# Performance work log

Measured on AMD Instinct MI355X. Metric: run time of the kernel, lower is better.

The kernel has to match this reference:

```python
import jax, jax.numpy as jnp
from jax import lax
import numpy as np

D_MODEL = 512
D_STATE = 16
D_CONV = 4
EXPAND = 2
D_INNER = EXPAND * D_MODEL  # 1024
DT_RANK = (D_MODEL + 15) // 16  # 32
FF_DIM = 1024
N_LAYERS = 2
B, L = 2, 2048


def setup_inputs() -> dict:
    key = jax.random.key(0)
    ks = jax.random.split(key, 16)
    s = 0.02
    x = jax.random.normal(ks[0], (B, L, D_MODEL), jnp.float32)
    in_proj_w = jax.random.normal(ks[1], (N_LAYERS, 2 * D_INNER, D_MODEL), jnp.float32) * s
    conv_w = jax.random.normal(ks[2], (N_LAYERS, D_INNER, D_CONV), jnp.float32) * 0.3
    conv_b = jax.random.normal(ks[3], (N_LAYERS, D_INNER), jnp.float32) * s
    x_proj_w = jax.random.normal(ks[4], (N_LAYERS, DT_RANK + 2 * D_STATE, D_INNER), jnp.float32) * s
    dt_proj_w = jax.random.normal(ks[5], (N_LAYERS, D_INNER, DT_RANK), jnp.float32) * s
    dt_proj_b = jax.random.normal(ks[6], (N_LAYERS, D_INNER), jnp.float32) * 0.5 - 4.0
    A_log = jnp.log(jnp.broadcast_to(jnp.arange(1, D_STATE + 1, dtype=jnp.float32), (N_LAYERS, D_INNER, D_STATE)))
    Dp = jnp.ones((N_LAYERS, D_INNER), jnp.float32)
    out_proj_w = jax.random.normal(ks[7], (N_LAYERS, D_MODEL, D_INNER), jnp.float32) * s
    mlp_w1 = jax.random.normal(ks[8], (FF_DIM, D_MODEL), jnp.float32) * s
    mlp_b1 = jnp.zeros((FF_DIM,), jnp.float32)
    mlp_w2 = jax.random.normal(ks[9], (D_MODEL, FF_DIM), jnp.float32) * s
    mlp_b2 = jnp.zeros((D_MODEL,), jnp.float32)
    return dict(x=x, in_proj_w=in_proj_w, conv_w=conv_w, conv_b=conv_b,
                x_proj_w=x_proj_w, dt_proj_w=dt_proj_w, dt_proj_b=dt_proj_b,
                A_log=A_log, Dp=Dp, out_proj_w=out_proj_w,
                mlp_w1=mlp_w1, mlp_b1=mlp_b1, mlp_w2=mlp_w2, mlp_b2=mlp_b2)


def _mamba_layer(x, ipw, cw, cb, xpw, dpw, dpb, Al, Dv, opw):
    # x: [B, L, d_model]
    b, l, _ = x.shape
    xz = jnp.einsum('bld,ed->ble', x, ipw)           # [B, L, 2*d_inner]
    xin, z = jnp.split(xz, 2, axis=-1)
    # causal depthwise conv1d (pad left d_conv-1)
    xc = jnp.transpose(xin, (0, 2, 1))               # [B, d_inner, L]
    xc = lax.conv_general_dilated(xc, cw[:, None, :], (1,), [(D_CONV - 1, 0)],
                                  feature_group_count=D_INNER)
    xin = jax.nn.silu(jnp.transpose(xc + cb[:, None], (0, 2, 1)))  # [B, L, d_inner]
    dbl = jnp.einsum('bld,ed->ble', xin, xpw)        # [B, L, dt_rank + 2*d_state]
    dt, Bm, Cm = jnp.split(dbl, [DT_RANK, DT_RANK + D_STATE], axis=-1)
    dt = jax.nn.softplus(jnp.einsum('blr,dr->bld', dt, dpw) + dpb)  # [B, L, d_inner]
    A = -jnp.exp(Al)                                  # [d_inner, d_state]
    dA = jnp.exp(dt[..., None] * A)                   # [B, L, d_inner, d_state]
    dBu = dt[..., None] * Bm[:, :, None, :] * xin[..., None]

    def step(h, inp):
        dA_t, dBu_t = inp
        h = dA_t * h + dBu_t
        return h, h

    h0 = jnp.zeros((b, D_INNER, D_STATE), x.dtype)
    _, hs = lax.scan(step, h0, (jnp.moveaxis(dA, 1, 0), jnp.moveaxis(dBu, 1, 0)))
    hs = jnp.moveaxis(hs, 0, 1)                       # [B, L, d_inner, d_state]
    y = jnp.einsum('blds,bls->bld', hs, Cm) + xin * Dv
    y = y * jax.nn.silu(z)
    return jnp.einsum('ble,de->bld', y, opw)


def reference(x, in_proj_w, conv_w, conv_b, x_proj_w, dt_proj_w, dt_proj_b,
              A_log, Dp, out_proj_w, mlp_w1, mlp_b1, mlp_w2, mlp_b2):
    residual = x
    for i in range(N_LAYERS):
        x = _mamba_layer(x, in_proj_w[i], conv_w[i], conv_b[i], x_proj_w[i],
                         dt_proj_w[i], dt_proj_b[i], A_log[i], Dp[i], out_proj_w[i])
    h = x + residual
    h = jax.nn.relu(jnp.einsum('bld,fd->blf', h, mlp_w1) + mlp_b1)  # dropout is identity in eval
    return jnp.einsum('blf,df->bld', h, mlp_w2) + mlp_b2
```

## Files before the change

kernel.cpp:

```cpp
#include <hip/hip_runtime.h>
#include <hip/hip_bf16.h>

#define BB 2
#define LL 2048
#define DMODEL 512
#define DSTATE 16
#define DINNER 1024
#define DTRANK 32
#define FFDIM 1024
#define MTOT (BB*LL)
#define SCL 64
#define NCC 32

typedef unsigned short u16;
typedef __attribute__((ext_vector_type(8))) short bf16x8;
typedef __attribute__((ext_vector_type(4))) float f32x4;

__device__ __forceinline__ float b2f(u16 u){
  unsigned v = ((unsigned)u) << 16; float f; __builtin_memcpy(&f, &v, 4); return f;
}
__device__ __forceinline__ u16 f2b(float f){
  unsigned u; __builtin_memcpy(&u, &f, 4);
  unsigned r = (u + 0x7FFFu + ((u >> 16) & 1u)) >> 16;
  return (u16)r;
}
__device__ __forceinline__ float siluf(float x){ return x / (1.f + __expf(-x)); }

__device__ __forceinline__ float ldin(const void* p, size_t i, int bf){
  if (bf) return b2f(((const u16*)p)[i]);
  return ((const float*)p)[i];
}
__device__ __forceinline__ void stout(void* p, size_t i, int bf, float v){
  if (bf) ((u16*)p)[i] = f2b(v);
  else    ((float*)p)[i] = v;
}

__device__ __forceinline__ int getbf(const void* dp){
  return (*(const unsigned*)dp == 0x3F803F80u) ? 1 : 0;
}

#define CVT_X   (MTOT*DMODEL)
#define CVT_IPW (2*2*DINNER*DMODEL)
#define CVT_XPW (2*64*DINNER)
#define CVT_DPW (2*DINNER*DTRANK)
#define CVT_OPW (2*DMODEL*DINNER)
#define CVT_W1  (FFDIM*DMODEL)
#define CVT_W2  (DMODEL*FFDIM)
#define CVT_TOT (CVT_X+CVT_IPW+CVT_XPW+CVT_DPW+CVT_OPW+CVT_W1+CVT_W2)
__global__ __launch_bounds__(256) void cvt_all_k(
    const void* __restrict__ x, const void* __restrict__ ipw,
    const void* __restrict__ xpw, const void* __restrict__ dpw,
    const void* __restrict__ opw, const void* __restrict__ w1,
    const void* __restrict__ w2, u16* __restrict__ dst,
    const void* __restrict__ dprobe)
{
  const int bf = getbf(dprobe);
  size_t i4 = ((size_t)blockIdx.x * 256 + threadIdx.x) * 4;
  if (i4 >= CVT_TOT) return;
  const void* src; size_t off = i4;
  if      (off < CVT_X)                       { src = x; }
  else if ((off -= CVT_X)   < CVT_IPW)        { src = ipw; }
  else if ((off -= CVT_IPW) < CVT_XPW)        { src = xpw; }
  else if ((off -= CVT_XPW) < CVT_DPW)        { src = dpw; }
  else if ((off -= CVT_DPW) < CVT_OPW)        { src = opw; }
  else if ((off -= CVT_OPW) < CVT_W1)         { src = w1; }
  else     { off -= CVT_W1;                     src = w2; }
  ushort4 o;
  if (bf) {
    o = *(const ushort4*)((const u16*)src + off);
  } else {
    float4 f = *(const float4*)((const float*)src + off);
    o.x = f2b(f.x); o.y = f2b(f.y); o.z = f2b(f.z); o.w = f2b(f.w);
  }
  *(ushort4*)(dst + i4) = o;
}

template<int CVT>
__device__ __forceinline__ bf16x8 ld8(const void* P, size_t gi, int bf){
  if (!CVT || bf) return *(const bf16x8*)((const u16*)P + gi);
  float4 f0 = *(const float4*)((const float*)P + gi);
  float4 f1 = *(const float4*)((const float*)P + gi + 4);
  union { u16 u[8]; bf16x8 v; } t;
  t.u[0]=f2b(f0.x); t.u[1]=f2b(f0.y); t.u[2]=f2b(f0.z); t.u[3]=f2b(f0.w);
  t.u[4]=f2b(f1.x); t.u[5]=f2b(f1.y); t.u[6]=f2b(f1.z); t.u[7]=f2b(f1.w);
  return t.v;
}

template<int ACT, int AIN, int CIN, int BM, int BN, int FST, int RESID>
__global__ __launch_bounds__(256) void gemm_mfma(
    const void* __restrict__ A, size_t aoff, int lda,
    const void* __restrict__ W, size_t woff,
    const void* __restrict__ bias, size_t boff,
    void* __restrict__ C, size_t coff, int ldc, int K,
    const void* __restrict__ xres, size_t xroff,
    const void* __restrict__ dprobe)
{
  const int bf = getbf(dprobe);
  constexpr int AL = BM / 64, WL = BN / 64;
  constexpr int CVTA = (!FST && AIN) ? 1 : 0;
  constexpr int CVTW = (!FST) ? 1 : 0;
  __shared__ __align__(16) u16 As[2][BM * 32];
  __shared__ __align__(16) u16 Ws[2][BN * 32];
  const int tid = threadIdx.x;
  const int row0 = blockIdx.y * BM, col0 = blockIdx.x * BN;
  const int wave = tid >> 6, lane = tid & 63;
  const int l15 = lane & 15, quad = lane >> 4;
  constexpr int WMT = (BM == 64) ? 1 : ((BN == 128) ? 4 : 2);
  const int mbase = (BM == 64) ? (wave * 16)
                  : ((BN == 128) ? (wave & 1) * 64 : wave * 32);
  const int nbase = (BM == 128 && BN == 128) ? (wave >> 1) * 64 : 0;

  const int rT = tid >> 2, csw = tid & 3;
  const int scg = csw ^ ((rT >> 1) & 3);
  const int lws = rT * 32 + csw * 8;
  const size_t ab0 = aoff + (size_t)(row0 + rT) * lda + scg * 8;
  const size_t wb0 = woff + (size_t)(col0 + rT) * K   + scg * 8;

  f32x4 acc[WMT][4];
#pragma unroll
  for (int i = 0; i < WMT; i++)
#pragma unroll
    for (int j = 0; j < 4; j++) acc[i][j] = (f32x4){0.f,0.f,0.f,0.f};

  const int NT = K >> 5;
  bf16x8 ra0[AL], rw0[WL], ra1[AL], rw1[WL];

#define GLOAD(RA, RW, T) do { const int k1_ = (T) * 32;                        \
  _Pragma("unroll") for (int i = 0; i < AL; i++)                               \
    RA[i] = ld8<CVTA>(A, ab0 + k1_ + (size_t)i * 64 * lda, bf);                \
  _Pragma("unroll") for (int i = 0; i < WL; i++)                               \
    RW[i] = ld8<CVTW>(W, wb0 + k1_ + (size_t)i * 64 * K, bf); } while (0)

#define GSTEP(RA, RW, T) do {                                                  \
  const int cur_ = (T) & 1;                                                    \
  _Pragma("unroll") for (int i = 0; i < AL; i++)                               \
    *(bf16x8*)&As[cur_][i * 2048 + lws] = RA[i];                               \
  _Pragma("unroll") for (int i = 0; i < WL; i++)                               \
    *(bf16x8*)&Ws[cur_][i * 2048 + lws] = RW[i];                               \
  if ((T) + 2 < NT) GLOAD(RA, RW, (T) + 2);                                    \
  __syncthreads();                                                             \
  bf16x8 af_[WMT], bf_[4];                                                     \
  _Pragma("unroll") for (int mt = 0; mt < WMT; mt++) {                         \
    int r_ = mbase + mt * 16 + l15;                                            \
    af_[mt] = *(const bf16x8*)&As[cur_][r_ * 32 + ((quad ^ ((r_ >> 1) & 3)) << 3)]; } \
  _Pragma("unroll") for (int nt = 0; nt < 4; nt++) {                           \
    int r_ = nbase + nt * 16 + l15;                                            \
    bf_[nt] = *(const bf16x8*)&Ws[cur_][r_ * 32 + ((quad ^ ((r_ >> 1) & 3)) << 3)]; } \
  _Pragma("unroll") for (int mt = 0; mt < WMT; mt++)                           \
    _Pragma("unroll") for (int nt = 0; nt < 4; nt++)                           \
      acc[mt][nt] = __builtin_amdgcn_mfma_f32_16x16x32_bf16(af_[mt], bf_[nt], acc[mt][nt], 0, 0, 0); \
} while (0)

  GLOAD(ra0, rw0, 0);
  if (NT > 1) GLOAD(ra1, rw1, 1);
  int t = 0;
  for (; t + 1 < NT; t += 2) { GSTEP(ra0, rw0, t); GSTEP(ra1, rw1, t + 1); }
  if (t < NT) GSTEP(ra0, rw0, t);
#undef GLOAD
#undef GSTEP

#pragma unroll
  for (int nt = 0; nt < 4; nt++) {
    int c = col0 + nbase + nt * 16 + l15;
    float bv = bias ? ldin(bias, boff + c, bf) : 0.f;
#pragma unroll
    for (int mt = 0; mt < WMT; mt++) {
      int rb = row0 + mbase + mt * 16 + quad * 4;
#pragma unroll
      for (int r = 0; r < 4; r++) {
        float v = acc[mt][nt][r] + bv;
        if (ACT == 1) v = fmaxf(v, 0.f) + __logf(1.f + __expf(-fabsf(v)));
        if (ACT == 2) v = fmaxf(v, 0.f);
        size_t ci = (size_t)(rb + r) * ldc + c;
        if (RESID) v += ldin(xres, xroff + ci, bf);
        if (CIN) stout(C, coff + ci, bf, v);
        else     ((u16*)C)[coff + ci] = f2b(v);
      }
    }
  }
}

__global__ __launch_bounds__(256) void conv_k(
    const u16* __restrict__ xz, const void* __restrict__ cw, size_t cwo,
    const void* __restrict__ cb, size_t cbo, u16* __restrict__ xc,
    const void* __restrict__ dprobe)
{
  const int bf = getbf(dprobe);
  int idx = blockIdx.x * 256 + threadIdx.x;
  int d = idx & 1023;
  int row = idx >> 10;
  int lb = row & (LL - 1);
  float acc = ldin(cb, cbo + d, bf);
#pragma unroll
  for (int k = 0; k < 4; k++) {
    int lk = lb - 3 + k;
    if (lk >= 0) acc += ldin(cw, cwo + d*4 + k, bf) * b2f(xz[(size_t)(row - 3 + k) * 2048 + d]);
  }
  xc[idx] = f2b(siluf(acc));
}

__global__ __launch_bounds__(256) void scan_A_k(
    const u16* __restrict__ dtp, int sdt, const u16* __restrict__ xc,
    const u16* __restrict__ dbl, const void* __restrict__ Alog, size_t alo,
    float* __restrict__ Pc, float* __restrict__ Sc, const void* __restrict__ dprobe)
{
  const int bf = getbf(dprobe);
  int bid = blockIdx.x;
  int b = bid >> 9;
  int c = (bid >> 4) & (NCC - 1);
  int g = bid & 15;
  int t = threadIdx.x;
  int dl = t >> 2, sq = t & 3;
  int d0 = g * 64, d = d0 + dl;
  int rowb = b * LL + c * SCL;

  __shared__ __align__(16) u16 dts[64 * 64];
  __shared__ __align__(16) u16 us[64 * 64];
  __shared__ __align__(16) float Bs[64 * 20];
#pragma unroll
  for (int p = 0; p < 2; p++) {
    int seg = p * 256 + t;
    int r = seg >> 3, c8 = (seg & 7) * 8;
    bf16x8 dv = *(const bf16x8*)&dtp[(size_t)(rowb + r) * sdt + d0 + c8];
    bf16x8 uv = *(const bf16x8*)&xc[(size_t)(rowb + r) * 1024 + d0 + c8];
    int coff = r >> 3, roff = r & 7;
#pragma unroll
    for (int i = 0; i < 8; i++) {
      int dd = c8 + i;
      int idx = dd * 64 + ((coff ^ (dd & 7)) << 3) + roff;
      dts[idx] = (u16)dv[i];
      us[idx]  = (u16)uv[i];
    }
  }
  if (t < 128) {
    int l = t >> 1, grp = t & 1;
    bf16x8 v = *(const bf16x8*)&dbl[(size_t)(rowb + l) * 64 + 32 + grp * 8];
    f32x4 f0 = {b2f((u16)v[0]), b2f((u16)v[1]), b2f((u16)v[2]), b2f((u16)v[3])};
    f32x4 f1 = {b2f((u16)v[4]), b2f((u16)v[5]), b2f((u16)v[6]), b2f((u16)v[7])};
    *(f32x4*)&Bs[l * 20 + grp * 8]     = f0;
    *(f32x4*)&Bs[l * 20 + grp * 8 + 4] = f1;
  }
  float Av[4];
#pragma unroll
  for (int j = 0; j < 4; j++)
    Av[j] = -__expf(ldin(Alog, alo + (size_t)d * DSTATE + sq * 4 + j, bf));
  __syncthreads();

  float h[4] = {0.f,0.f,0.f,0.f}, P[4] = {1.f,1.f,1.f,1.f};
  for (int cc = 0; cc < 8; cc++) {
    int base = dl * 64 + ((cc ^ (dl & 7)) << 3);
    bf16x8 dt8 = *(const bf16x8*)&dts[base];
    bf16x8 u8  = *(const bf16x8*)&us[base];
#pragma unroll
    for (int i = 0; i < 8; i++) {
      int l = cc * 8 + i;
      float dtv = b2f((u16)dt8[i]);
      float uv  = b2f((u16)u8[i]);
      float dtu = dtv * uv;
      f32x4 B4 = *(const f32x4*)&Bs[l * 20 + sq * 4];
#pragma unroll
      for (int j = 0; j < 4; j++) {
        float dA = __expf(dtv * Av[j]);
        h[j] = dA * h[j] + dtu * B4[j];
        P[j] *= dA;
      }
    }
  }
  size_t o = (((size_t)b * DINNER + d) * NCC + c) * DSTATE + sq * 4;
  *(f32x4*)&Pc[o] = (f32x4){P[0], P[1], P[2], P[3]};
  *(f32x4*)&Sc[o] = (f32x4){h[0], h[1], h[2], h[3]};
}

__global__ __launch_bounds__(256) void scan_B_k(
    float* __restrict__ Pc, const float* __restrict__ Sc)
{
  int idx = blockIdx.x * 256 + threadIdx.x;
  int bd = idx >> 4, s = idx & 15;
  float h = 0.f;
  for (int c = 0; c < NCC; c++) {
    size_t o = ((size_t)bd * NCC + c) * DSTATE + s;
    float P = Pc[o], S = Sc[o];
    Pc[o] = h;
    h = P * h + S;
  }
}

__global__ __launch_bounds__(256) void scan_C_k(
    u16* __restrict__ dtp, int sdt, const u16* __restrict__ xz,
    const u16* __restrict__ xc,
    const u16* __restrict__ dbl, const void* __restrict__ Alog, size_t alo,
    const void* __restrict__ Dpt, size_t dpo, const float* __restrict__ Hinit,
    const void* __restrict__ dprobe)
{
  const int bf = getbf(dprobe);
  int bid = blockIdx.x;
  int b = bid >> 9;
  int c = (bid >> 4) & (NCC - 1);
  int g = bid & 15;
  int t = threadIdx.x;
  int dl = t >> 2, sq = t & 3;
  int d0 = g * 64, d = d0 + dl;
  int rowb = b * LL + c * SCL;

  __shared__ __align__(16) u16 dts[64 * 64];
  __shared__ __align__(16) u16 us[64 * 64];
  __shared__ __align__(16) u16 outs[64 * 64];
  __shared__ __align__(16) float BCs[64 * 36];
#pragma unroll
  for (int p = 0; p < 2; p++) {
    int seg = p * 256 + t;
    int r = seg >> 3, c8 = (seg & 7) * 8;
    bf16x8 dv = *(const bf16x8*)&dtp[(size_t)(rowb + r) * sdt + d0 + c8];
    bf16x8 uv = *(const bf16x8*)&xc[(size_t)(rowb + r) * 1024 + d0 + c8];
    int coff = r >> 3, roff = r & 7;
#pragma unroll
    for (int i = 0; i < 8; i++) {
      int dd = c8 + i;
      int idx = dd * 64 + ((coff ^ (dd & 7)) << 3) + roff;
      dts[idx] = (u16)dv[i];
      us[idx]  = (u16)uv[i];
    }
  }
  {
    int l = t >> 2, grp = t & 3;
    bf16x8 v = *(const bf16x8*)&dbl[(size_t)(rowb + l) * 64 + 32 + grp * 8];
    f32x4 f0 = {b2f((u16)v[0]), b2f((u16)v[1]), b2f((u16)v[2]), b2f((u16)v[3])};
    f32x4 f1 = {b2f((u16)v[4]), b2f((u16)v[5]), b2f((u16)v[6]), b2f((u16)v[7])};
    *(f32x4*)&BCs[l * 36 + grp * 8]     = f0;
    *(f32x4*)&BCs[l * 36 + grp * 8 + 4] = f1;
  }
  float Av[4];
#pragma unroll
  for (int j = 0; j < 4; j++)
    Av[j] = -__expf(ldin(Alog, alo + (size_t)d * DSTATE + sq * 4 + j, bf));
  float Dv = ldin(Dpt, dpo + d, bf);
  float h[4];
  size_t o = (((size_t)b * DINNER + d) * NCC + c) * DSTATE + sq * 4;
  f32x4 h4 = *(const f32x4*)&Hinit[o];
  h[0] = h4[0]; h[1] = h4[1]; h[2] = h4[2]; h[3] = h4[3];
  __syncthreads();

  for (int cc = 0; cc < 8; cc++) {
    int base = dl * 64 + ((cc ^ (dl & 7)) << 3);
    bf16x8 dt8 = *(const bf16x8*)&dts[base];
    bf16x8 u8  = *(const bf16x8*)&us[base];
#pragma unroll
    for (int i = 0; i < 8; i++) {
      int l = cc * 8 + i;
      float dtv = b2f((u16)dt8[i]);
      float uv  = b2f((u16)u8[i]);
      float dtu = dtv * uv;
      f32x4 B4 = *(const f32x4*)&BCs[l * 36 + sq * 4];
      f32x4 C4 = *(const f32x4*)&BCs[l * 36 + 16 + sq * 4];
      float y = 0.f;
#pragma unroll
      for (int j = 0; j < 4; j++) {
        float dA = __expf(dtv * Av[j]);
        h[j] = dA * h[j] + dtu * B4[j];
        y += h[j] * C4[j];
      }
      y += __shfl_xor(y, 1);
      y += __shfl_xor(y, 2);
      if (sq == 0) outs[l * 64 + dl] = f2b(y + uv * Dv);
    }
  }
  __syncthreads();
#pragma unroll
  for (int p = 0; p < 2; p++) {
    int seg = p * 256 + t;
    int r = seg >> 3, c8 = (seg & 7) * 8;
    bf16x8 yv = *(const bf16x8*)&outs[r * 64 + c8];
    bf16x8 zv = *(const bf16x8*)&xz[(size_t)(rowb + r) * 2048 + 1024 + d0 + c8];
    bf16x8 ov;
#pragma unroll
    for (int i = 0; i < 8; i++) {
      float z = b2f((u16)zv[i]);
      ov[i] = (short)f2b(b2f((u16)yv[i]) * siluf(z));
    }
    *(bf16x8*)&dtp[(size_t)(rowb + r) * sdt + d0 + c8] = ov;
  }
}

extern "C" void kernel_launch(void* const* d_in, const int* in_sizes, int n_in,
                              void* d_out, int out_size, void* d_ws, size_t ws_size,
                              hipStream_t stream) {
  const void* x_in = d_in[0];
  const void* ipw  = d_in[1];
  const void* cw   = d_in[2];
  const void* cb   = d_in[3];
  const void* xpw  = d_in[4];
  const void* dpw  = d_in[5];
  const void* dpb  = d_in[6];
  const void* Alog = d_in[7];
  const void* Dpt  = d_in[8];
  const void* opw  = d_in[9];
  const void* w1   = d_in[10];
  const void* b1   = d_in[11];
  const void* w2   = d_in[12];
  const void* b2   = d_in[13];

  const bool full = ws_size >= (size_t)64 * 1024 * 1024;

  if (full) {
    float* Pc = (float*)((char*)d_ws + 64);
    float* Sc = Pc + (size_t)BB*DINNER*NCC*DSTATE;
    u16* p = (u16*)(Sc + (size_t)BB*DINNER*NCC*DSTATE);
    u16* x16   = p;  p += (size_t)CVT_X;
    u16* ipw16 = p;  p += (size_t)CVT_IPW;
    u16* xpw16 = p;  p += (size_t)CVT_XPW;
    u16* dpw16 = p;  p += (size_t)CVT_DPW;
    u16* opw16 = p;  p += (size_t)CVT_OPW;
    u16* w116  = p;  p += (size_t)CVT_W1;
    u16* w216  = p;  p += (size_t)CVT_W2;
    u16* xz    = p;  p += (size_t)MTOT*2*DINNER;
    u16* xc    = p;  p += (size_t)MTOT*DINNER;
    u16* dty   = p;  p += (size_t)MTOT*DINNER;
    u16* dbl   = p;
    u16* bx = xc;
    u16* resid = xz;
    u16* hid = xz + (size_t)4*1024*1024;

    cvt_all_k<<<(CVT_TOT/4 + 255)/256, 256, 0, stream>>>(
        x_in, ipw, xpw, dpw, opw, w1, w2, x16, Dpt);

    for (int layer = 0; layer < 2; layer++) {
      size_t ipw_o = (size_t)layer*2*DINNER*DMODEL;
      size_t cw_o  = (size_t)layer*DINNER*4,  cb_o = (size_t)layer*DINNER;
      size_t xpw_o = (size_t)layer*64*DINNER, dpw_o = (size_t)layer*DINNER*DTRANK;
      size_t dpb_o = (size_t)layer*DINNER,    al_o = (size_t)layer*DINNER*DSTATE;
      size_t dp_o  = (size_t)layer*DINNER,    opw_o = (size_t)layer*DMODEL*DINNER;
      const u16* xsrc = (layer == 0) ? x16 : bx;
      gemm_mfma<0,0,0,128,128,1,0><<<dim3(16, 32), 256, 0, stream>>>(
          xsrc, 0, DMODEL, ipw16, ipw_o, nullptr, 0, xz, 0, 2048, DMODEL,
          nullptr, 0, Dpt);
      conv_k<<<MTOT*DINNER/256, 256, 0, stream>>>(xz, cw, cw_o, cb, cb_o, xc, Dpt);
      gemm_mfma<0,0,0,64,64,1,0><<<dim3(1, 64), 256, 0, stream>>>(
          xc, 0, DINNER, xpw16, xpw_o, nullptr, 0, dbl, 0, 64, DINNER,
          nullptr, 0, Dpt);
      gemm_mfma<1,0,0,64,64,1,0><<<dim3(16, 64), 256, 0, stream>>>(
          dbl, 0, 64, dpw16, dpw_o, dpb, dpb_o, dty, 0, 1024, DTRANK,
          nullptr, 0, Dpt);
      scan_A_k<<<BB*NCC*16, 256, 0, stream>>>(dty, 1024, xc, dbl, Alog, al_o, Pc, Sc, Dpt);
      scan_B_k<<<BB*64, 256, 0, stream>>>(Pc, Sc);
      scan_C_k<<<BB*NCC*16, 256, 0, stream>>>(dty, 1024, xz, xc, dbl, Alog, al_o,
                                              Dpt, dp_o, Pc, Dpt);
      if (layer == 0)
        gemm_mfma<0,0,0,64,64,1,0><<<dim3(8, 64), 256, 0, stream>>>(
            dty, 0, 1024, opw16, opw_o, nullptr, 0, bx, 0, DMODEL, DINNER,
            nullptr, 0, Dpt);
      else
        gemm_mfma<0,0,0,64,64,1,1><<<dim3(8, 64), 256, 0, stream>>>(
            dty, 0, 1024, opw16, opw_o, nullptr, 0, resid, 0, DMODEL, DINNER,
            x_in, 0, Dpt);
    }
    gemm_mfma<2,0,0,64,64,1,0><<<dim3(16, 64), 256, 0, stream>>>(
        resid, 0, DMODEL, w116, 0, b1, 0, hid, 0, FFDIM, DMODEL,
        nullptr, 0, Dpt);
    gemm_mfma<0,0,1,64,64,1,0><<<dim3(8, 64), 256, 0, stream>>>(
        hid, 0, FFDIM, w216, 0, b2, 0, d_out, 0, DMODEL, FFDIM,
        nullptr, 0, Dpt);
  } else {
    float* Pc = (float*)((char*)d_ws + 64);
    float* Sc = Pc + (size_t)DINNER*NCC*DSTATE;
    u16* p = (u16*)(Sc + (size_t)DINNER*NCC*DSTATE);
    u16* xz  = p;  p += (size_t)LL*2*DINNER;
    u16* xc  = p;  p += (size_t)LL*DINNER;
    u16* bxF = p;  p += (size_t)MTOT*DMODEL;
    u16* dbl = p;
    u16* hid = xz + (size_t)2*1024*1024;

    for (int layer = 0; layer < 2; layer++) {
      size_t ipw_o = (size_t)layer*2*DINNER*DMODEL;
      size_t cw_o  = (size_t)layer*DINNER*4,  cb_o = (size_t)layer*DINNER;
      size_t xpw_o = (size_t)layer*64*DINNER, dpw_o = (size_t)layer*DINNER*DTRANK;
      size_t dpb_o = (size_t)layer*DINNER,    al_o = (size_t)layer*DINNER*DSTATE;
      size_t dp_o  = (size_t)layer*DINNER,    opw_o = (size_t)layer*DMODEL*DINNER;
      for (int b = 0; b < BB; b++) {
        size_t ro = (size_t)b * LL * DMODEL;
        if (layer == 0)
          gemm_mfma<0,1,0,128,128,0,0><<<dim3(16, 16), 256, 0, stream>>>(
              x_in, ro, DMODEL, ipw, ipw_o, nullptr, 0, xz, 0, 2048, DMODEL,
              nullptr, 0, Dpt);
        else
          gemm_mfma<0,0,0,128,128,0,0><<<dim3(16, 16), 256, 0, stream>>>(
              bxF, ro, DMODEL, ipw, ipw_o, nullptr, 0, xz, 0, 2048, DMODEL,
              nullptr, 0, Dpt);
        conv_k<<<LL*DINNER/256, 256, 0, stream>>>(xz, cw, cw_o, cb, cb_o, xc, Dpt);
        gemm_mfma<0,0,0,64,64,0,0><<<dim3(1, 32), 256, 0, stream>>>(
            xc, 0, DINNER, xpw, xpw_o, nullptr, 0, dbl, 0, 64, DINNER,
            nullptr, 0, Dpt);
        gemm_mfma<1,0,0,64,64,0,0><<<dim3(16, 32), 256, 0, stream>>>(
            dbl, 0, 64, dpw, dpw_o, dpb, dpb_o, xz, 0, 2048, DTRANK,
            nullptr, 0, Dpt);
        scan_A_k<<<NCC*16, 256, 0, stream>>>(xz, 2048, xc, dbl, Alog, al_o, Pc, Sc, Dpt);
        scan_B_k<<<64, 256, 0, stream>>>(Pc, Sc);
        scan_C_k<<<NCC*16, 256, 0, stream>>>(xz, 2048, xz, xc, dbl, Alog, al_o,
                                             Dpt, dp_o, Pc, Dpt);
        if (layer == 0)
          gemm_mfma<0,0,0,64,64,0,0><<<dim3(8, 32), 256, 0, stream>>>(
              xz, 0, 2048, opw, opw_o, nullptr, 0, bxF, ro, DMODEL, DINNER,
              nullptr, 0, Dpt);
        else
          gemm_mfma<0,0,0,64,64,0,1><<<dim3(8, 32), 256, 0, stream>>>(
              xz, 0, 2048, opw, opw_o, nullptr, 0, bxF, ro, DMODEL, DINNER,
              x_in, ro, Dpt);
      }
    }
    for (int b = 0; b < BB; b++) {
      size_t ro = (size_t)b * LL * DMODEL;
      gemm_mfma<2,0,0,64,64,0,0><<<dim3(16, 32), 256, 0, stream>>>(
          bxF, ro, DMODEL, w1, 0, b1, 0, hid, 0, FFDIM, DMODEL,
          nullptr, 0, Dpt);
      gemm_mfma<0,0,1,64,64,0,0><<<dim3(8, 32), 256, 0, stream>>>(
          hid, 0, FFDIM, w2, 0, b2, 0, d_out, ro, DMODEL, FFDIM,
          nullptr, 0, Dpt);
    }
  }
}
```

Measured before the change: 357.0 us.

## Fuse dt_proj GEMM and softplus into scan kernels, vectorize conv, drop x conversion

Result: faster. 328.9 us (-7.9%).

```diff
diff --git a/kernel.cpp b/kernel.cpp
--- a/kernel.cpp
+++ b/kernel.cpp
@@ -25,6 +25,9 @@
   return (u16)r;
 }
 __device__ __forceinline__ float siluf(float x){ return x / (1.f + __expf(-x)); }
+__device__ __forceinline__ float softplusf(float v){
+  return fmaxf(v, 0.f) + __logf(1.f + __expf(-fabsf(v)));
+}
 
 __device__ __forceinline__ float ldin(const void* p, size_t i, int bf){
   if (bf) return b2f(((const u16*)p)[i]);
@@ -37,42 +40,6 @@
 
 __device__ __forceinline__ int getbf(const void* dp){
   return (*(const unsigned*)dp == 0x3F803F80u) ? 1 : 0;
-}
-
-#define CVT_X   (MTOT*DMODEL)
-#define CVT_IPW (2*2*DINNER*DMODEL)
-#define CVT_XPW (2*64*DINNER)
-#define CVT_DPW (2*DINNER*DTRANK)
-#define CVT_OPW (2*DMODEL*DINNER)
-#define CVT_W1  (FFDIM*DMODEL)
-#define CVT_W2  (DMODEL*FFDIM)
-#define CVT_TOT (CVT_X+CVT_IPW+CVT_XPW+CVT_DPW+CVT_OPW+CVT_W1+CVT_W2)
-__global__ __launch_bounds__(256) void cvt_all_k(
-    const void* __restrict__ x, const void* __restrict__ ipw,
-    const void* __restrict__ xpw, const void* __restrict__ dpw,
-    const void* __restrict__ opw, const void* __restrict__ w1,
-    const void* __restrict__ w2, u16* __restrict__ dst,
-    const void* __restrict__ dprobe)
-{
-  const int bf = getbf(dprobe);
-  size_t i4 = ((size_t)blockIdx.x * 256 + threadIdx.x) * 4;
-  if (i4 >= CVT_TOT) return;
-  const void* src; size_t off = i4;
-  if      (off < CVT_X)                       { src = x; }
-  else if ((off -= CVT_X)   < CVT_IPW)        { src = ipw; }
-  else if ((off -= CVT_IPW) < CVT_XPW)        { src = xpw; }
-  else if ((off -= CVT_XPW) < CVT_DPW)        { src = dpw; }
-  else if ((off -= CVT_DPW) < CVT_OPW)        { src = opw; }
-  else if ((off -= CVT_OPW) < CVT_W1)         { src = w1; }
-  else     { off -= CVT_W1;                     src = w2; }
-  ushort4 o;
-  if (bf) {
-    o = *(const ushort4*)((const u16*)src + off);
-  } else {
-    float4 f = *(const float4*)((const float*)src + off);
-    o.x = f2b(f.x); o.y = f2b(f.y); o.z = f2b(f.z); o.w = f2b(f.w);
-  }
-  *(ushort4*)(dst + i4) = o;
 }
 
 template<int CVT>
@@ -86,7 +53,45 @@
   return t.v;
 }
 
-template<int ACT, int AIN, int CIN, int BM, int BN, int FST, int RESID>
+#define CVT_IPW (2*2*DINNER*DMODEL)
+#define CVT_XPW (2*64*DINNER)
+#define CVT_DPW (2*DINNER*DTRANK)
+#define CVT_OPW (2*DMODEL*DINNER)
+#define CVT_W1  (FFDIM*DMODEL)
+#define CVT_W2  (DMODEL*FFDIM)
+#define CVT_CW  (2*DINNER*4)
+#define CVT_CB  (2*DINNER)
+#define CVT_TOT (CVT_IPW+CVT_XPW+CVT_DPW+CVT_OPW+CVT_W1+CVT_W2+CVT_CW+CVT_CB)
+__global__ __launch_bounds__(256) void cvt_all_k(
+    const void* __restrict__ ipw, const void* __restrict__ xpw,
+    const void* __restrict__ dpw, const void* __restrict__ opw,
+    const void* __restrict__ w1, const void* __restrict__ w2,
+    const void* __restrict__ cw, const void* __restrict__ cb,
+    u16* __restrict__ dst, const void* __restrict__ dprobe)
+{
+  const int bf = getbf(dprobe);
+  size_t i4 = ((size_t)blockIdx.x * 256 + threadIdx.x) * 4;
+  if (i4 >= CVT_TOT) return;
+  const void* src; size_t off = i4;
+  if      (off < CVT_IPW)                     { src = ipw; }
+  else if ((off -= CVT_IPW) < CVT_XPW)        { src = xpw; }
+  else if ((off -= CVT_XPW) < CVT_DPW)        { src = dpw; }
+  else if ((off -= CVT_DPW) < CVT_OPW)        { src = opw; }
+  else if ((off -= CVT_OPW) < CVT_W1)         { src = w1; }
+  else if ((off -= CVT_W1)  < CVT_W2)         { src = w2; }
+  else if ((off -= CVT_W2)  < CVT_CW)         { src = cw; }
+  else     { off -= CVT_CW;                     src = cb; }
+  ushort4 o;
+  if (bf) {
+    o = *(const ushort4*)((const u16*)src + off);
+  } else {
+    float4 f = *(const float4*)((const float*)src + off);
+    o.x = f2b(f.x); o.y = f2b(f.y); o.z = f2b(f.z); o.w = f2b(f.w);
+  }
+  *(ushort4*)(dst + i4) = o;
+}
+
+template<int ACT, int CVA, int CVW, int CIN, int BM, int BN, int RESID>
 __global__ __launch_bounds__(256) void gemm_mfma(
     const void* __restrict__ A, size_t aoff, int lda,
     const void* __restrict__ W, size_t woff,
@@ -97,8 +102,6 @@
 {
   const int bf = getbf(dprobe);
   constexpr int AL = BM / 64, WL = BN / 64;
-  constexpr int CVTA = (!FST && AIN) ? 1 : 0;
-  constexpr int CVTW = (!FST) ? 1 : 0;
   __shared__ __align__(16) u16 As[2][BM * 32];
   __shared__ __align__(16) u16 Ws[2][BN * 32];
   const int tid = threadIdx.x;
@@ -127,9 +130,9 @@
 
 #define GLOAD(RA, RW, T) do { const int k1_ = (T) * 32;                        \
   _Pragma("unroll") for (int i = 0; i < AL; i++)                               \
-    RA[i] = ld8<CVTA>(A, ab0 + k1_ + (size_t)i * 64 * lda, bf);                \
+    RA[i] = ld8<CVA>(A, ab0 + k1_ + (size_t)i * 64 * lda, bf);                 \
   _Pragma("unroll") for (int i = 0; i < WL; i++)                               \
-    RW[i] = ld8<CVTW>(W, wb0 + k1_ + (size_t)i * 64 * K, bf); } while (0)
+    RW[i] = ld8<CVW>(W, wb0 + k1_ + (size_t)i * 64 * K, bf); } while (0)
 
 #define GSTEP(RA, RW, T) do {                                                  \
   const int cur_ = (T) & 1;                                                    \
@@ -169,7 +172,7 @@
 #pragma unroll
       for (int r = 0; r < 4; r++) {
         float v = acc[mt][nt][r] + bv;
-        if (ACT == 1) v = fmaxf(v, 0.f) + __logf(1.f + __expf(-fabsf(v)));
+        if (ACT == 1) v = softplusf(v);
         if (ACT == 2) v = fmaxf(v, 0.f);
         size_t ci = (size_t)(rb + r) * ldc + c;
         if (RESID) v += ldin(xres, xroff + ci, bf);
@@ -180,29 +183,70 @@
   }
 }
 
+template<int FST>
 __global__ __launch_bounds__(256) void conv_k(
     const u16* __restrict__ xz, const void* __restrict__ cw, size_t cwo,
     const void* __restrict__ cb, size_t cbo, u16* __restrict__ xc,
     const void* __restrict__ dprobe)
 {
-  const int bf = getbf(dprobe);
-  int idx = blockIdx.x * 256 + threadIdx.x;
-  int d = idx & 1023;
-  int row = idx >> 10;
-  int lb = row & (LL - 1);
-  float acc = ldin(cb, cbo + d, bf);
-#pragma unroll
-  for (int k = 0; k < 4; k++) {
-    int lk = lb - 3 + k;
-    if (lk >= 0) acc += ldin(cw, cwo + d*4 + k, bf) * b2f(xz[(size_t)(row - 3 + k) * 2048 + d]);
-  }
-  xc[idx] = f2b(siluf(acc));
-}
-
+  if (FST) {
+    const u16* cw16 = (const u16*)cw;
+    const u16* cb16 = (const u16*)cb;
+    int idx8 = (blockIdx.x * 256 + threadIdx.x) * 8;
+    int d8 = idx8 & 1023;
+    int row = idx8 >> 10;
+    int lb = row & (LL - 1);
+    bf16x8 cwv0 = *(const bf16x8*)&cw16[cwo + d8*4];
+    bf16x8 cwv1 = *(const bf16x8*)&cw16[cwo + d8*4 + 8];
+    bf16x8 cwv2 = *(const bf16x8*)&cw16[cwo + d8*4 + 16];
+    bf16x8 cwv3 = *(const bf16x8*)&cw16[cwo + d8*4 + 24];
+    bf16x8 cbv  = *(const bf16x8*)&cb16[cbo + d8];
+    bf16x8 xv0 = (bf16x8){0,0,0,0,0,0,0,0}, xv1 = xv0, xv2 = xv0, xv3 = xv0;
+    if (lb >= 3) xv0 = *(const bf16x8*)&xz[(size_t)(row - 3) * 2048 + d8];
+    if (lb >= 2) xv1 = *(const bf16x8*)&xz[(size_t)(row - 2) * 2048 + d8];
+    if (lb >= 1) xv2 = *(const bf16x8*)&xz[(size_t)(row - 1) * 2048 + d8];
+    xv3 = *(const bf16x8*)&xz[(size_t)row * 2048 + d8];
+    bf16x8 ov;
+#pragma unroll
+    for (int i = 0; i < 8; i++) {
+      float acc = b2f((u16)cbv[i]);
+      int c0 = i * 4;
+      float w0 = b2f((u16)((c0 < 8) ? cwv0[c0 & 7] : (c0 < 16) ? cwv1[c0 & 7] : (c0 < 24) ? cwv2[c0 & 7] : cwv3[c0 & 7]));
+      float w1_ = b2f((u16)(((c0+1) < 8) ? cwv0[(c0+1) & 7] : ((c0+1) < 16) ? cwv1[(c0+1) & 7] : ((c0+1) < 24) ? cwv2[(c0+1) & 7] : cwv3[(c0+1) & 7]));
+      float w2_ = b2f((u16)(((c0+2) < 8) ? cwv0[(c0+2) & 7] : ((c0+2) < 16) ? cwv1[(c0+2) & 7] : ((c0+2) < 24) ? cwv2[(c0+2) & 7] : cwv3[(c0+2) & 7]));
+      float w3_ = b2f((u16)(((c0+3) < 8) ? cwv0[(c0+3) & 7] : ((c0+3) < 16) ? cwv1[(c0+3) & 7] : ((c0+3) < 24) ? cwv2[(c0+3) & 7] : cwv3[(c0+3) & 7]));
+      acc += w0 * b2f((u16)xv0[i]);
+      acc += w1_ * b2f((u16)xv1[i]);
+      acc += w2_ * b2f((u16)xv2[i]);
+      acc += w3_ * b2f((u16)xv3[i]);
+      ov[i] = (short)f2b(siluf(acc));
+    }
+    *(bf16x8*)&xc[idx8] = ov;
+  } else {
+    const int bf = getbf(dprobe);
+    int idx = blockIdx.x * 256 + threadIdx.x;
+    int d = idx & 1023;
+    int row = idx >> 10;
+    int lb = row & (LL - 1);
+    float acc = ldin(cb, cbo + d, bf);
+#pragma unroll
+    for (int k = 0; k < 4; k++) {
+      int lk = lb - 3 + k;
+      if (lk >= 0) acc += ldin(cw, cwo + d*4 + k, bf) * b2f(xz[(size_t)(row - 3 + k) * 2048 + d]);
+    }
+    xc[idx] = f2b(siluf(acc));
+  }
+}
+
+template<int CVW>
 __global__ __launch_bounds__(256) void scan_A_k(
-    const u16* __restrict__ dtp, int sdt, const u16* __restrict__ xc,
-    const u16* __restrict__ dbl, const void* __restrict__ Alog, size_t alo,
-    float* __restrict__ Pc, float* __restrict__ Sc, const void* __restrict__ dprobe)
+    const u16* __restrict__ xc,
+    const u16* __restrict__ dbl,
+    const void* __restrict__ dpwp, size_t dpwo,
+    const void* __restrict__ dpbp, size_t dpbo,
+    const void* __restrict__ Alog, size_t alo,
+    float* __restrict__ Pc, float* __restrict__ Sc,
+    const void* __restrict__ dprobe)
 {
   const int bf = getbf(dprobe);
   int bid = blockIdx.x;
@@ -217,19 +261,26 @@
   __shared__ __align__(16) u16 dts[64 * 64];
   __shared__ __align__(16) u16 us[64 * 64];
   __shared__ __align__(16) float Bs[64 * 20];
+  u16* dbls = dts;
+  u16* dpws = dts + 64 * 32;
+
+  {
+    int r = t >> 2, c8 = (t & 3) * 8;
+    *(bf16x8*)&dbls[r * 32 + c8] =
+        *(const bf16x8*)&dbl[(size_t)(rowb + r) * 64 + c8];
+    *(bf16x8*)&dpws[r * 32 + c8] =
+        ld8<CVW>(dpwp, dpwo + (size_t)(d0 + r) * DTRANK + c8, bf);
+  }
 #pragma unroll
   for (int p = 0; p < 2; p++) {
     int seg = p * 256 + t;
     int r = seg >> 3, c8 = (seg & 7) * 8;
-    bf16x8 dv = *(const bf16x8*)&dtp[(size_t)(rowb + r) * sdt + d0 + c8];
     bf16x8 uv = *(const bf16x8*)&xc[(size_t)(rowb + r) * 1024 + d0 + c8];
     int coff = r >> 3, roff = r & 7;
 #pragma unroll
     for (int i = 0; i < 8; i++) {
       int dd = c8 + i;
-      int idx = dd * 64 + ((coff ^ (dd & 7)) << 3) + roff;
-      dts[idx] = (u16)dv[i];
-      us[idx]  = (u16)uv[i];
+      us[dd * 64 + ((coff ^ (dd & 7)) << 3) + roff] = (u16)uv[i];
     }
   }
   if (t < 128) {
@@ -244,6 +295,36 @@
 #pragma unroll
   for (int j = 0; j < 4; j++)
     Av[j] = -__expf(ldin(Alog, alo + (size_t)d * DSTATE + sq * 4 + j, bf));
+  __syncthreads();
+
+  {
+    int wv = t >> 6, lane = t & 63;
+    int fl = lane & 15, qd = lane >> 4;
+    bf16x8 afr  = *(const bf16x8*)&dbls[(wv * 16 + fl) * 32 + qd * 8];
+    bf16x8 bfr0 = *(const bf16x8*)&dpws[(fl)      * 32 + qd * 8];
+    bf16x8 bfr1 = *(const bf16x8*)&dpws[(16 + fl) * 32 + qd * 8];
+    bf16x8 bfr2 = *(const bf16x8*)&dpws[(32 + fl) * 32 + qd * 8];
+    bf16x8 bfr3 = *(const bf16x8*)&dpws[(48 + fl) * 32 + qd * 8];
+    __syncthreads();
+    f32x4 zz = {0.f, 0.f, 0.f, 0.f};
+    f32x4 a0 = __builtin_amdgcn_mfma_f32_16x16x32_bf16(afr, bfr0, zz, 0, 0, 0);
+    f32x4 a1 = __builtin_amdgcn_mfma_f32_16x16x32_bf16(afr, bfr1, zz, 0, 0, 0);
+    f32x4 a2 = __builtin_amdgcn_mfma_f32_16x16x32_bf16(afr, bfr2, zz, 0, 0, 0);
+    f32x4 a3 = __builtin_amdgcn_mfma_f32_16x16x32_bf16(afr, bfr3, zz, 0, 0, 0);
+    int lc = wv * 2 + (qd >> 1);
+    int off = (qd & 1) * 4;
+#define DTWR(AN, NT) do {                                                      \
+    int dd_ = (NT) * 16 + fl;                                                  \
+    float bvv_ = ldin(dpbp, dpbo + d0 + dd_, bf);                              \
+    ushort4 pk_;                                                               \
+    pk_.x = f2b(softplusf(AN[0] + bvv_));                                      \
+    pk_.y = f2b(softplusf(AN[1] + bvv_));                                      \
+    pk_.z = f2b(softplusf(AN[2] + bvv_));                                      \
+    pk_.w = f2b(softplusf(AN[3] + bvv_));                                      \
+    *(ushort4*)&dts[dd_ * 64 + ((lc ^ (dd_ & 7)) << 3) + off] = pk_; } while (0)
+    DTWR(a0, 0); DTWR(a1, 1); DTWR(a2, 2); DTWR(a3, 3);
+#undef DTWR
+  }
   __syncthreads();
 
   float h[4] = {0.f,0.f,0.f,0.f}, P[4] = {1.f,1.f,1.f,1.f};
@@ -285,10 +366,14 @@
   }
 }
 
+template<int CVW>
 __global__ __launch_bounds__(256) void scan_C_k(
     u16* __restrict__ dtp, int sdt, const u16* __restrict__ xz,
     const u16* __restrict__ xc,
-    const u16* __restrict__ dbl, const void* __restrict__ Alog, size_t alo,
+    const u16* __restrict__ dbl,
+    const void* __restrict__ dpwp, size_t dpwo,
+    const void* __restrict__ dpbp, size_t dpbo,
+    const void* __restrict__ Alog, size_t alo,
     const void* __restrict__ Dpt, size_t dpo, const float* __restrict__ Hinit,
     const void* __restrict__ dprobe)
 {
@@ -306,19 +391,26 @@
   __shared__ __align__(16) u16 us[64 * 64];
   __shared__ __align__(16) u16 outs[64 * 64];
   __shared__ __align__(16) float BCs[64 * 36];
+  u16* dbls = dts;
+  u16* dpws = dts + 64 * 32;
+
+  {
+    int r = t >> 2, c8 = (t & 3) * 8;
+    *(bf16x8*)&dbls[r * 32 + c8] =
+        *(const bf16x8*)&dbl[(size_t)(rowb + r) * 64 + c8];
+    *(bf16x8*)&dpws[r * 32 + c8] =
+        ld8<CVW>(dpwp, dpwo + (size_t)(d0 + r) * DTRANK + c8, bf);
+  }
 #pragma unroll
   for (int p = 0; p < 2; p++) {
     int seg = p * 256 + t;
     int r = seg >> 3, c8 = (seg & 7) * 8;
-    bf16x8 dv = *(const bf16x8*)&dtp[(size_t)(rowb + r) * sdt + d0 + c8];
     bf16x8 uv = *(const bf16x8*)&xc[(size_t)(rowb + r) * 1024 + d0 + c8];
     int coff = r >> 3, roff = r & 7;
 #pragma unroll
     for (int i = 0; i < 8; i++) {
       int dd = c8 + i;
-      int idx = dd * 64 + ((coff ^ (dd & 7)) << 3) + roff;
-      dts[idx] = (u16)dv[i];
-      us[idx]  = (u16)uv[i];
+      us[dd * 64 + ((coff ^ (dd & 7)) << 3) + roff] = (u16)uv[i];
     }
   }
   {
@@ -338,6 +430,36 @@
   size_t o = (((size_t)b * DINNER + d) * NCC + c) * DSTATE + sq * 4;
   f32x4 h4 = *(const f32x4*)&Hinit[o];
   h[0] = h4[0]; h[1] = h4[1]; h[2] = h4[2]; h[3] = h4[3];
+  __syncthreads();
+
+  {
+    int wv = t >> 6, lane = t & 63;
+    int fl = lane & 15, qd = lane >> 4;
+    bf16x8 afr  = *(const bf16x8*)&dbls[(wv * 16 + fl) * 32 + qd * 8];
+    bf16x8 bfr0 = *(const bf16x8*)&dpws[(fl)      * 32 + qd * 8];
+    bf16x8 bfr1 = *(const bf16x8*)&dpws[(16 + fl) * 32 + qd * 8];
+    bf16x8 bfr2 = *(const bf16x8*)&dpws[(32 + fl) * 32 + qd * 8];
+    bf16x8 bfr3 = *(const bf16x8*)&dpws[(48 + fl) * 32 + qd * 8];
+    __syncthreads();
+    f32x4 zz = {0.f, 0.f, 0.f, 0.f};
+    f32x4 a0 = __builtin_amdgcn_mfma_f32_16x16x32_bf16(afr, bfr0, zz, 0, 0, 0);
+    f32x4 a1 = __builtin_amdgcn_mfma_f32_16x16x32_bf16(afr, bfr1, zz, 0, 0, 0);
+    f32x4 a2 = __builtin_amdgcn_mfma_f32_16x16x32_bf16(afr, bfr2, zz, 0, 0, 0);
+    f32x4 a3 = __builtin_amdgcn_mfma_f32_16x16x32_bf16(afr, bfr3, zz, 0, 0, 0);
+    int lc = wv * 2 + (qd >> 1);
+    int off = (qd & 1) * 4;
+#define DTWR(AN, NT) do {                                                      \
+    int dd_ = (NT) * 16 + fl;                                                  \
+    float bvv_ = ldin(dpbp, dpbo + d0 + dd_, bf);                              \
+    ushort4 pk_;                                                               \
+    pk_.x = f2b(softplusf(AN[0] + bvv_));                                      \
+    pk_.y = f2b(softplusf(AN[1] + bvv_));                                      \
+    pk_.z = f2b(softplusf(AN[2] + bvv_));                                      \
+    pk_.w = f2b(softplusf(AN[3] + bvv_));                                      \
+    *(ushort4*)&dts[dd_ * 64 + ((lc ^ (dd_ & 7)) << 3) + off] = pk_; } while (0)
+    DTWR(a0, 0); DTWR(a1, 1); DTWR(a2, 2); DTWR(a3, 3);
+#undef DTWR
+  }
   __syncthreads();
 
   for (int cc = 0; cc < 8; cc++) {
@@ -405,13 +527,15 @@
     float* Pc = (float*)((char*)d_ws + 64);
     float* Sc = Pc + (size_t)BB*DINNER*NCC*DSTATE;
     u16* p = (u16*)(Sc + (size_t)BB*DINNER*NCC*DSTATE);
-    u16* x16   = p;  p += (size_t)CVT_X;
+    u16* cvt0  = p;
     u16* ipw16 = p;  p += (size_t)CVT_IPW;
     u16* xpw16 = p;  p += (size_t)CVT_XPW;
     u16* dpw16 = p;  p += (size_t)CVT_DPW;
     u16* opw16 = p;  p += (size_t)CVT_OPW;
     u16* w116  = p;  p += (size_t)CVT_W1;
     u16* w216  = p;  p += (size_t)CVT_W2;
+    u16* cw16  = p;  p += (size_t)CVT_CW;
+    u16* cb16  = p;  p += (size_t)CVT_CB;
     u16* xz    = p;  p += (size_t)MTOT*2*DINNER;
     u16* xc    = p;  p += (size_t)MTOT*DINNER;
     u16* dty   = p;  p += (size_t)MTOT*DINNER;
@@ -421,7 +545,7 @@
     u16* hid = xz + (size_t)4*1024*1024;
 
     cvt_all_k<<<(CVT_TOT/4 + 255)/256, 256, 0, stream>>>(
-        x_in, ipw, xpw, dpw, opw, w1, w2, x16, Dpt);
+        ipw, xpw, dpw, opw, w1, w2, cw, cb, cvt0, Dpt);
 
     for (int layer = 0; layer < 2; layer++) {
       size_t ipw_o = (size_t)layer*2*DINNER*DMODEL;
@@ -429,34 +553,38 @@
       size_t xpw_o = (size_t)layer*64*DINNER, dpw_o = (size_t)layer*DINNER*DTRANK;
       size_t dpb_o = (size_t)layer*DINNER,    al_o = (size_t)layer*DINNER*DSTATE;
       size_t dp_o  = (size_t)layer*DINNER,    opw_o = (size_t)layer*DMODEL*DINNER;
-      const u16* xsrc = (layer == 0) ? x16 : bx;
-      gemm_mfma<0,0,0,128,128,1,0><<<dim3(16, 32), 256, 0, stream>>>(
-          xsrc, 0, DMODEL, ipw16, ipw_o, nullptr, 0, xz, 0, 2048, DMODEL,
-          nullptr, 0, Dpt);
-      conv_k<<<MTOT*DINNER/256, 256, 0, stream>>>(xz, cw, cw_o, cb, cb_o, xc, Dpt);
-      gemm_mfma<0,0,0,64,64,1,0><<<dim3(1, 64), 256, 0, stream>>>(
+      if (layer == 0)
+        gemm_mfma<0,1,0,0,128,128,0><<<dim3(16, 32), 256, 0, stream>>>(
+            x_in, 0, DMODEL, ipw16, ipw_o, nullptr, 0, xz, 0, 2048, DMODEL,
+            nullptr, 0, Dpt);
+      else
+        gemm_mfma<0,0,0,0,128,128,0><<<dim3(16, 32), 256, 0, stream>>>(
+            bx, 0, DMODEL, ipw16, ipw_o, nullptr, 0, xz, 0, 2048, DMODEL,
+            nullptr, 0, Dpt);
+      conv_k<1><<<MTOT*DINNER/2048, 256, 0, stream>>>(
+          xz, cw16, cw_o, cb16, cb_o, xc, Dpt);
+      gemm_mfma<0,0,0,0,64,64,0><<<dim3(1, 64), 256, 0, stream>>>(
           xc, 0, DINNER, xpw16, xpw_o, nullptr, 0, dbl, 0, 64, DINNER,
           nullptr, 0, Dpt);
-      gemm_mfma<1,0,0,64,64,1,0><<<dim3(16, 64), 256, 0, stream>>>(
-          dbl, 0, 64, dpw16, dpw_o, dpb, dpb_o, dty, 0, 1024, DTRANK,
-          nullptr, 0, Dpt);
-      scan_A_k<<<BB*NCC*16, 256, 0, stream>>>(dty, 1024, xc, dbl, Alog, al_o, Pc, Sc, Dpt);
+      scan_A_k<0><<<BB*NCC*16, 256, 0, stream>>>(
+          xc, dbl, dpw16, dpw_o, dpb, dpb_o, Alog, al_o, Pc, Sc, Dpt);
       scan_B_k<<<BB*64, 256, 0, stream>>>(Pc, Sc);
-      scan_C_k<<<BB*NCC*16, 256, 0, stream>>>(dty, 1024, xz, xc, dbl, Alog, al_o,
-                                              Dpt, dp_o, Pc, Dpt);
+      scan_C_k<0><<<BB*NCC*16, 256, 0, stream>>>(
+          dty, 1024, xz, xc, dbl, dpw16, dpw_o, dpb, dpb_o, Alog, al_o,
+          Dpt, dp_o, Pc, Dpt);
       if (layer == 0)
-        gemm_mfma<0,0,0,64,64,1,0><<<dim3(8, 64), 256, 0, stream>>>(
+        gemm_mfma<0,0,0,0,64,64,0><<<dim3(8, 64), 256, 0, stream>>>(
             dty, 0, 1024, opw16, opw_o, nullptr, 0, bx, 0, DMODEL, DINNER,
             nullptr, 0, Dpt);
       else
-        gemm_mfma<0,0,0,64,64,1,1><<<dim3(8, 64), 256, 0, stream>>>(
+        gemm_mfma<0,0,0,0,64,64,1><<<dim3(8, 64), 256, 0, stream>>>(
             dty, 0, 1024, opw16, opw_o, nullptr, 0, resid, 0, DMODEL, DINNER,
             x_in, 0, Dpt);
     }
-    gemm_mfma<2,0,0,64,64,1,0><<<dim3(16, 64), 256, 0, stream>>>(
+    gemm_mfma<2,0,0,0,64,64,0><<<dim3(16, 64), 256, 0, stream>>>(
         resid, 0, DMODEL, w116, 0, b1, 0, hid, 0, FFDIM, DMODEL,
         nullptr, 0, Dpt);
-    gemm_mfma<0,0,1,64,64,1,0><<<dim3(8, 64), 256, 0, stream>>>(
+    gemm_mfma<0,0,0,1,64,64,0><<<dim3(8, 64), 256, 0, stream>>>(
         hid, 0, FFDIM, w216, 0, b2, 0, d_out, 0, DMODEL, FFDIM,
         nullptr, 0, Dpt);
   } else {
@@ -478,40 +606,39 @@
       for (int b = 0; b < BB; b++) {
         size_t ro = (size_t)b * LL * DMODEL;
         if (layer == 0)
-          gemm_mfma<0,1,0,128,128,0,0><<<dim3(16, 16), 256, 0, stream>>>(
+          gemm_mfma<0,1,1,0,128,128,0><<<dim3(16, 16), 256, 0, stream>>>(
               x_in, ro, DMODEL, ipw, ipw_o, nullptr, 0, xz, 0, 2048, DMODEL,
               nullptr, 0, Dpt);
         else
-          gemm_mfma<0,0,0,128,128,0,0><<<dim3(16, 16), 256, 0, stream>>>(
+          gemm_mfma<0,0,1,0,128,128,0><<<dim3(16, 16), 256, 0, stream>>>(
               bxF, ro, DMODEL, ipw, ipw_o, nullptr, 0, xz, 0, 2048, DMODEL,
               nullptr, 0, Dpt);
-        conv_k<<<LL*DINNER/256, 256, 0, stream>>>(xz, cw, cw_o, cb, cb_o, xc, Dpt);
-        gemm_mfma<0,0,0,64,64,0,0><<<dim3(1, 32), 256, 0, stream>>>(
+        conv_k<0><<<LL*DINNER/256, 256, 0, stream>>>(xz, cw, cw_o, cb, cb_o, xc, Dpt);
+        gemm_mfma<0,0,1,0,64,64,0><<<dim3(1, 32), 256, 0, stream>>>(
             xc, 0, DINNER, xpw, xpw_o, nullptr, 0, dbl, 0, 64, DINNER,
             nullptr, 0, Dpt);
-        gemm_mfma<1,0,0,64,64,0,0><<<dim3(16, 32), 256, 0, stream>>>(
-            dbl, 0, 64, dpw, dpw_o, dpb, dpb_o, xz, 0, 2048, DTRANK,
-            nullptr, 0, Dpt);
-        scan_A_k<<<NCC*16, 256, 0, stream>>>(xz, 2048, xc, dbl, Alog, al_o, Pc, Sc, Dpt);
+        scan_A_k<1><<<NCC*16, 256, 0, stream>>>(
+            xc, dbl, dpw, dpw_o, dpb, dpb_o, Alog, al_o, Pc, Sc, Dpt);
         scan_B_k<<<64, 256, 0, stream>>>(Pc, Sc);
-        scan_C_k<<<NCC*16, 256, 0, stream>>>(xz, 2048, xz, xc, dbl, Alog, al_o,
-                                             Dpt, dp_o, Pc, Dpt);
+        scan_C_k<1><<<NCC*16, 256, 0, stream>>>(
+            xz, 2048, xz, xc, dbl, dpw, dpw_o, dpb, dpb_o, Alog, al_o,
+            Dpt, dp_o, Pc, Dpt);
         if (layer == 0)
-          gemm_mfma<0,0,0,64,64,0,0><<<dim3(8, 32), 256, 0, stream>>>(
+          gemm_mfma<0,0,1,0,64,64,0><<<dim3(8, 32), 256, 0, stream>>>(
               xz, 0, 2048, opw, opw_o, nullptr, 0, bxF, ro, DMODEL, DINNER,
               nullptr, 0, Dpt);
         else
-          gemm_mfma<0,0,0,64,64,0,1><<<dim3(8, 32), 256, 0, stream>>>(
+          gemm_mfma<0,0,1,0,64,64,1><<<dim3(8, 32), 256, 0, stream>>>(
               xz, 0, 2048, opw, opw_o, nullptr, 0, bxF, ro, DMODEL, DINNER,
               x_in, ro, Dpt);
       }
     }
     for (int b = 0; b < BB; b++) {
       size_t ro = (size_t)b * LL * DMODEL;
-      gemm_mfma<2,0,0,64,64,0,0><<<dim3(16, 32), 256, 0, stream>>>(
+      gemm_mfma<2,0,1,0,64,64,0><<<dim3(16, 32), 256, 0, stream>>>(
           bxF, ro, DMODEL, w1, 0, b1, 0, hid, 0, FFDIM, DMODEL,
           nullptr, 0, Dpt);
-      gemm_mfma<0,0,1,64,64,0,0><<<dim3(8, 32), 256, 0, stream>>>(
+      gemm_mfma<0,0,1,1,64,64,0><<<dim3(8, 32), 256, 0, stream>>>(
           hid, 0, FFDIM, w2, 0, b2, 0, d_out, ro, DMODEL, FFDIM,
           nullptr, 0, Dpt);
     }
```
